# Kernel tuning notes

Measured on AMD Instinct MI355X. Metric: run time of the kernel, lower is better.

## Reference

```python
import jax, jax.numpy as jnp
import numpy as np
import math

CH_IN = 256
NUM_HEADS = 4
HEAD_CH = 64
NUM_GROUPS = 32
EPS = 1e-5


def setup_inputs() -> dict:
    key = jax.random.key(0)
    ks = jax.random.split(key, 12)
    B, C, H, W = 16, CH_IN, 32, 32
    s_in = 1.0 / math.sqrt(C)  # conv 1x1 fan_in init scale
    s_proj = 1.0 / math.sqrt(NUM_HEADS * HEAD_CH)
    return {
        "x": jax.random.normal(ks[0], (B, C, H, W), dtype=jnp.float32),
        "gamma": jnp.ones((C,), dtype=jnp.float32),
        "beta": jnp.zeros((C,), dtype=jnp.float32),
        # per-head 1x1 convs stacked: [num_heads, head_ch, ch_in]
        "wq": jax.random.normal(ks[1], (NUM_HEADS, HEAD_CH, C), dtype=jnp.float32) * s_in,
        "bq": jax.random.normal(ks[2], (NUM_HEADS, HEAD_CH), dtype=jnp.float32) * s_in,
        "wk": jax.random.normal(ks[3], (NUM_HEADS, HEAD_CH, C), dtype=jnp.float32) * s_in,
        "bk": jax.random.normal(ks[4], (NUM_HEADS, HEAD_CH), dtype=jnp.float32) * s_in,
        "wv": jax.random.normal(ks[5], (NUM_HEADS, HEAD_CH, C), dtype=jnp.float32) * s_in,
        "bv": jax.random.normal(ks[6], (NUM_HEADS, HEAD_CH), dtype=jnp.float32) * s_in,
        # output 1x1 conv: [ch_in, num_heads*head_ch]
        "wproj": jax.random.normal(ks[7], (C, NUM_HEADS * HEAD_CH), dtype=jnp.float32) * s_proj,
        "bproj": jax.random.normal(ks[8], (C,), dtype=jnp.float32) * s_proj,
    }


def group_norm(x, gamma, beta):
    B, C, H, W = x.shape
    xg = x.reshape(B, NUM_GROUPS, C // NUM_GROUPS, H, W)
    mean = xg.mean(axis=(2, 3, 4), keepdims=True)
    var = xg.var(axis=(2, 3, 4), keepdims=True)
    xn = (xg - mean) * jax.lax.rsqrt(var + EPS)
    xn = xn.reshape(B, C, H, W)
    return xn * gamma[None, :, None, None] + beta[None, :, None, None]


def reference(x, gamma, beta, wq, bq, wk, bk, wv, bv, wproj, bproj):
    B, C, H, W = x.shape
    L = H * W
    h = group_norm(x, gamma, beta)
    hf = h.reshape(B, C, L)  # [B, C, L]
    # per-head 1x1 convs as batched channel contractions: [B, n_heads, d, L]
    q = jnp.einsum("bcl,ndc->bndl", hf, wq) + bq[None, :, :, None]
    k = jnp.einsum("bcl,ndc->bndl", hf, wk) + bk[None, :, :, None]
    v = jnp.einsum("bcl,ndc->bndl", hf, wv) + bv[None, :, :, None]
    scale = 1.0 / math.sqrt(HEAD_CH)
    scores = jnp.einsum("bndl,bndm->bnlm", q, k) * scale  # [B, n, L, L]
    attn = jax.nn.softmax(scores, axis=-1)
    out = jnp.einsum("bnlm,bndm->bndl", attn, v)  # [B, n, d, L]
    out = out.reshape(B, NUM_HEADS * HEAD_CH, L)  # concat heads along channels
    proj = jnp.einsum("bel,ce->bcl", out, wproj) + bproj[None, :, None]
    return proj.reshape(B, C, H, W) + x
```

## Files before the change

### kernel.cpp

```cpp
#include <hip/hip_runtime.h>
#include <hip/hip_bf16.h>
#include <stdint.h>


typedef __hip_bfloat16 bf16;
typedef __attribute__((ext_vector_type(8))) short short8;
typedef __attribute__((ext_vector_type(4))) float float4v;
typedef __attribute__((ext_vector_type(16))) float float16v;

#if __has_builtin(__builtin_amdgcn_exp2f)
#define EXP2F(x) __builtin_amdgcn_exp2f(x)
#else
#define EXP2F(x) exp2f(x)
#endif

__device__ __forceinline__ float max3f(float a, float b, float c) {
  return fmaxf(fmaxf(a, b), c);
}

__device__ __forceinline__ int qk_fidx(int d, int l) {
  return ((((l >> 5) * 4 + (d >> 4)) * 64 + ((d >> 3) & 1) * 32 + (l & 31)) << 3) + (d & 7);
}
__device__ __forceinline__ int v_fidx(int d, int l) {
  return (((((((l >> 5) * 2 + (d >> 5)) * 2 + ((l >> 4) & 1)) * 2 + ((l >> 3) & 1)) * 32) + (d & 31)) << 3) + (l & 7);
}

__global__ __launch_bounds__(256) void stats_wpack_kernel(
    const float* __restrict__ x, float2* __restrict__ stats,
    const float* __restrict__ wq, const float* __restrict__ wk,
    const float* __restrict__ wv, const float* __restrict__ wp,
    bf16* __restrict__ Wb, bf16* __restrict__ Pb) {
  if (blockIdx.x < 512) {
    int b = blockIdx.x >> 5, g = blockIdx.x & 31;
    const float* xp = x + (size_t)(b * 256 + g * 8) * 1024;
    float s = 0.f, ss = 0.f;
    for (int i = threadIdx.x; i < 8192; i += 256) {
      float v = xp[i]; s += v; ss += v * v;
    }
    #pragma unroll
    for (int o = 32; o; o >>= 1) { s += __shfl_down(s, o); ss += __shfl_down(ss, o); }
    __shared__ float red[2][4];
    int wid = threadIdx.x >> 6;
    if ((threadIdx.x & 63) == 0) { red[0][wid] = s; red[1][wid] = ss; }
    __syncthreads();
    if (threadIdx.x == 0) {
      s  = red[0][0] + red[0][1] + red[0][2] + red[0][3];
      ss = red[1][0] + red[1][1] + red[1][2] + red[1][3];
      float mean = s * (1.f / 8192.f);
      float var  = ss * (1.f / 8192.f) - mean * mean;
      stats[blockIdx.x] = make_float2(mean, rsqrtf(var + 1e-5f));
    }
  } else {
    int i = (blockIdx.x - 512) * 256 + threadIdx.x;
    if (i < 196608) {
      int r = i >> 8, c = i & 255;
      const float* src = (r < 256) ? wq : (r < 512) ? wk : wv;
      Wb[i] = __float2bfloat16(src[(r & 255) * 256 + c]);
    } else {
      int j = i - 196608;
      Pb[j] = __float2bfloat16(wp[j]);
    }
  }
}

__global__ __launch_bounds__(256) void gemm_qkv_fused(
    const float* __restrict__ x, const float* __restrict__ gamma,
    const float* __restrict__ beta, const float2* __restrict__ stats,
    const bf16* __restrict__ Wb,
    const float* __restrict__ bq, const float* __restrict__ bk,
    const float* __restrict__ bv,
    bf16* __restrict__ qkv, size_t qkv_bstride, int b_off) {
  __shared__ bf16 As[128][40];
  __shared__ bf16 Bs[128][40];
  __shared__ float2 ssh[256];
  int zb = blockIdx.z, b = zb + b_off;
  int m0 = blockIdx.y * 128, l0 = blockIdx.x * 128;
  const float* xb = x + (size_t)b * 262144;
  int tid = threadIdx.x, lane = tid & 63, wave = tid >> 6;
  int l16 = lane & 15, quad = lane >> 4;
  int mi0 = (wave & 1) * 4, nj0 = (wave >> 1) * 4;

  {
    float2 st = stats[b * 32 + (tid >> 3)];
    float sc = st.y * gamma[tid];
    ssh[tid] = make_float2(sc, beta[tid] - st.x * sc);
  }

  float4v acc[4][4];
  #pragma unroll
  for (int i = 0; i < 4; i++)
    #pragma unroll
    for (int j = 0; j < 4; j++) acc[i][j] = (float4v){0.f, 0.f, 0.f, 0.f};

  for (int kc = 0; kc < 8; kc++) {
    __syncthreads();
    #pragma unroll
    for (int it = 0; it < 2; it++) {
      int s = it * 256 + tid;
      int mm = s >> 2, kk = (s & 3) * 8;
      *(short8*)&As[mm][kk] = *(const short8*)&Wb[(size_t)(m0 + mm) * 256 + kc * 32 + kk];
    }
    #pragma unroll
    for (int it = 0; it < 16; it++) {
      int i = it * 256 + tid;
      int cl = i >> 7, ll = i & 127;
      float2 sh = ssh[kc * 32 + cl];
      float v = xb[(size_t)(kc * 32 + cl) * 1024 + l0 + ll];
      Bs[ll][cl] = __float2bfloat16(v * sh.x + sh.y);
    }
    __syncthreads();
    short8 af[4], bfr[4];
    #pragma unroll
    for (int i = 0; i < 4; i++) af[i]  = *(const short8*)&As[(mi0 + i) * 16 + l16][quad * 8];
    #pragma unroll
    for (int j = 0; j < 4; j++) bfr[j] = *(const short8*)&Bs[(nj0 + j) * 16 + l16][quad * 8];
    #pragma unroll
    for (int i = 0; i < 4; i++)
      #pragma unroll
      for (int j = 0; j < 4; j++)
        acc[i][j] = __builtin_amdgcn_mfma_f32_16x16x32_bf16(af[i], bfr[j], acc[i][j], 0, 0, 0);
  }

  bf16* Cp = qkv + (size_t)zb * qkv_bstride;
  int sec = m0 >> 8;
  const float* bptr = (sec == 0) ? bq : (sec == 1) ? bk : bv;
  if (sec <= 1) {
    float osc = (sec == 0) ? 0.125f * 1.4426950408889634f : 1.0f;
    bf16* Tp = Cp + sec * 262144;
    #pragma unroll
    for (int i = 0; i < 4; i++) {
      int rrb = (m0 & 255) + (mi0 + i) * 16 + quad * 4;
      int nh = rrb >> 6, d0 = rrb & 63;
      float b0 = bptr[rrb], b1 = bptr[rrb + 1], b2 = bptr[rrb + 2], b3 = bptr[rrb + 3];
      bf16* Tph = Tp + nh * 65536;
      #pragma unroll
      for (int j = 0; j < 4; j++) {
        int l = l0 + (nj0 + j) * 16 + l16;
        bf16 h0 = __float2bfloat16((acc[i][j][0] + b0) * osc);
        bf16 h1 = __float2bfloat16((acc[i][j][1] + b1) * osc);
        bf16 h2 = __float2bfloat16((acc[i][j][2] + b2) * osc);
        bf16 h3 = __float2bfloat16((acc[i][j][3] + b3) * osc);
        uint2 pk;
        pk.x = (unsigned int)*(unsigned short*)&h0 |
               ((unsigned int)*(unsigned short*)&h1 << 16);
        pk.y = (unsigned int)*(unsigned short*)&h2 |
               ((unsigned int)*(unsigned short*)&h3 << 16);
        *(uint2*)&Tph[qk_fidx(d0, l)] = pk;
      }
    }
  } else {
    bf16* Vfp = Cp + 524288;
    #pragma unroll
    for (int i = 0; i < 4; i++)
      #pragma unroll
      for (int r = 0; r < 4; r++) {
        int rr = (m0 & 255) + (mi0 + i) * 16 + quad * 4 + r;
        float bias = bptr[rr];
        int nh = rr >> 6, d = rr & 63;
        bf16* Vfh = Vfp + nh * 65536;
        #pragma unroll
        for (int j = 0; j < 4; j++) {
          int l = l0 + (nj0 + j) * 16 + l16;
          Vfh[v_fidx(d, l)] = __float2bfloat16(acc[i][j][r] + bias);
        }
      }
  }
}

__global__ __launch_bounds__(256) void attn_kernel(
    const bf16* __restrict__ qkv, bf16* __restrict__ oT,
    size_t qkv_bstride, size_t o_bstride) {
  __shared__ __align__(16) float OB[2][2][2176];
  __shared__ float mL[2][2][32], lL[2][2][32];

  int zb, n, gg;
  {
    int f = blockIdx.x + (blockIdx.y << 4) + (blockIdx.z << 6);
    if (gridDim.z == 16) {
      int c = f & 7, r = f >> 3;
      int h = (r >> 4) * 8 + c;
      zb = h >> 2; n = h & 3; gg = r & 15;
    } else {
      zb = blockIdx.z; n = blockIdx.y; gg = blockIdx.x;
    }
  }
  const bf16* base = qkv + (size_t)zb * qkv_bstride;
  const bf16* Qf = base + n * 65536;
  const bf16* Kf = base + 262144 + n * 65536;
  const bf16* Vf = base + 524288 + n * 65536;
  int tid = threadIdx.x;
  int lane = tid & 63, wave = tid >> 6;
  int l31 = lane & 31, hb2 = lane >> 5;
  int qt = wave >> 1, half = wave & 1;
  int g = gg * 2 + qt;
  int q0 = g << 5;

  short8 qb[4];
  #pragma unroll
  for (int ds = 0; ds < 4; ds++)
    qb[ds] = *(const short8*)&Qf[(((g * 4 + ds) << 6) + lane) << 3];

  float m_run = -1e30f, l_run = 0.f;
  float16v oaccT[2];
  #pragma unroll
  for (int dh = 0; dh < 2; dh++)
    #pragma unroll
    for (int r = 0; r < 16; r++) oaccT[dh][r] = 0.f;

  auto swp = [&](unsigned int a, unsigned int b, unsigned int& o0, unsigned int& o1) {
#if __has_builtin(__builtin_amdgcn_permlane32_swap)
    auto rr = __builtin_amdgcn_permlane32_swap((int)a, (int)b, false, false);
    o0 = (unsigned int)rr[0]; o1 = (unsigned int)rr[1];
#else
    unsigned int sa = (unsigned int)__shfl_xor((int)a, 32, 64);
    unsigned int sb = (unsigned int)__shfl_xor((int)b, 32, 64);
    o0 = hb2 ? sb : a;
    o1 = hb2 ? b : sa;
#endif
  };

  int k0 = half << 4;
  for (int kt = k0; kt < k0 + 16; kt++) {
    short8 kf[4];
    #pragma unroll
    for (int ds = 0; ds < 4; ds++)
      kf[ds] = *(const short8*)&Kf[(((kt * 4 + ds) << 6) + lane) << 3];
    short8 vf[2][2];
    #pragma unroll
    for (int dh = 0; dh < 2; dh++)
      #pragma unroll
      for (int s = 0; s < 2; s++)
        vf[dh][s] = *(const short8*)&Vf[((((kt * 2 + dh) * 2 + s) << 6) + lane) << 3];

    float16v sacc;
    #pragma unroll
    for (int r = 0; r < 16; r++) sacc[r] = 0.f;
    #pragma unroll
    for (int ds = 0; ds < 4; ds++)
      sacc = __builtin_amdgcn_mfma_f32_32x32x16_bf16(kf[ds], qb[ds], sacc, 0, 0, 0);

    float a0 = max3f(sacc[0], sacc[1], sacc[2]);
    float a1 = max3f(sacc[3], sacc[4], sacc[5]);
    float a2 = max3f(sacc[6], sacc[7], sacc[8]);
    float a3 = max3f(sacc[9], sacc[10], sacc[11]);
    float a4 = max3f(sacc[12], sacc[13], sacc[14]);
    float cmax = fmaxf(max3f(a0, a1, a2), max3f(a3, a4, sacc[15]));
    cmax = fmaxf(cmax, __shfl_xor(cmax, 32, 64));

    if (__any(cmax > m_run + 8.f)) {
      float mnew = fmaxf(m_run, cmax);
      float alpha = EXP2F(m_run - mnew);
      #pragma unroll
      for (int dh = 0; dh < 2; dh++)
        #pragma unroll
        for (int r = 0; r < 16; r++) oaccT[dh][r] *= alpha;
      l_run *= alpha;
      m_run = mnew;
    }

    float p[16];
    #pragma unroll
    for (int r = 0; r < 16; r++) p[r] = EXP2F(sacc[r] - m_run);
    float s0 = (p[0] + p[1]) + (p[2] + p[3]);
    float s1 = (p[4] + p[5]) + (p[6] + p[7]);
    float s2 = (p[8] + p[9]) + (p[10] + p[11]);
    float s3 = (p[12] + p[13]) + (p[14] + p[15]);
    float psum = (s0 + s1) + (s2 + s3);
    psum += __shfl_xor(psum, 32, 64);
    l_run += psum;

    unsigned int w[8];
    #pragma unroll
    for (int i = 0; i < 8; i++) {
      unsigned int pk;
      asm("v_cvt_pk_bf16_f32 %0, %1, %2" : "=v"(pk) : "v"(p[2 * i]), "v"(p[2 * i + 1]));
      w[i] = pk;
    }
    short8 pb[2];
    {
      unsigned int o0, o1, o2, o3;
      swp(w[0], w[2], o0, o2); swp(w[1], w[3], o1, o3);
      unsigned int* pw = (unsigned int*)&pb[0];
      pw[0] = o0; pw[1] = o1; pw[2] = o2; pw[3] = o3;
      swp(w[4], w[6], o0, o2); swp(w[5], w[7], o1, o3);
      pw = (unsigned int*)&pb[1];
      pw[0] = o0; pw[1] = o1; pw[2] = o2; pw[3] = o3;
    }

    #pragma unroll
    for (int dh = 0; dh < 2; dh++)
      #pragma unroll
      for (int s = 0; s < 2; s++)
        oaccT[dh] = __builtin_amdgcn_mfma_f32_32x32x16_bf16(vf[dh][s], pb[s], oaccT[dh], 0, 0, 0);
  }

  #pragma unroll
  for (int dh = 0; dh < 2; dh++)
    #pragma unroll
    for (int rq = 0; rq < 4; rq++) {
      float4v t = {oaccT[dh][4 * rq], oaccT[dh][4 * rq + 1],
                   oaccT[dh][4 * rq + 2], oaccT[dh][4 * rq + 3]};
      *(float4v*)&OB[half][qt][l31 * 68 + dh * 32 + 8 * rq + 4 * hb2] = t;
    }
  if (hb2 == 0) { mL[half][qt][l31] = m_run; lL[half][qt][l31] = l_run; }
  __syncthreads();

  bf16* op = oT + (size_t)zb * o_bstride + n * 64;
  const float* OA = OB[0][qt];
  const float* OBp = OB[1][qt];
  #pragma unroll
  for (int i = 0; i < 16; i++) {
    int q = (half << 4) + i;
    float mA = mL[0][qt][q], mB = mL[1][qt][q];
    float lA = lL[0][qt][q], lB = lL[1][qt][q];
    float ms = fmaxf(mA, mB);
    float eA = EXP2F(mA - ms), eB = EXP2F(mB - ms);
    float inv = 1.f / (lA * eA + lB * eB);
    float va = OA[q * 68 + lane], vb = OBp[q * 68 + lane];
    float o = (va * eA + vb * eB) * inv;
    op[(size_t)(q0 + q) * 256 + lane] = __float2bfloat16(o);
  }
}

__global__ __launch_bounds__(256) void gemm_proj_mfma(
    const bf16* __restrict__ Pb, const bf16* __restrict__ oT,
    const float* __restrict__ bproj, const float* __restrict__ x,
    float* __restrict__ out, int b_off, size_t o_bstride) {
  __shared__ bf16 As[128][40];
  __shared__ bf16 Bs[128][40];
  int zb = blockIdx.z, b = zb + b_off;
  int m0 = blockIdx.y * 128, l0 = blockIdx.x * 128;
  const bf16* ob = oT + (size_t)zb * o_bstride;
  int tid = threadIdx.x, lane = tid & 63, wave = tid >> 6;
  int l16 = lane & 15, quad = lane >> 4;
  int mi0 = (wave & 1) * 4, nj0 = (wave >> 1) * 4;
  float4v acc[4][4];
  #pragma unroll
  for (int i = 0; i < 4; i++)
    #pragma unroll
    for (int j = 0; j < 4; j++) acc[i][j] = (float4v){0.f, 0.f, 0.f, 0.f};

  for (int kc = 0; kc < 8; kc++) {
    __syncthreads();
    #pragma unroll
    for (int it = 0; it < 2; it++) {
      int s = it * 256 + tid;
      int mm = s >> 2, kk = (s & 3) * 8;
      *(short8*)&As[mm][kk] = *(const short8*)&Pb[(size_t)(m0 + mm) * 256 + kc * 32 + kk];
      *(short8*)&Bs[mm][kk] = *(const short8*)&ob[(size_t)(l0 + mm) * 256 + kc * 32 + kk];
    }
    __syncthreads();
    short8 af[4], bfr[4];
    #pragma unroll
    for (int i = 0; i < 4; i++) af[i]  = *(const short8*)&As[(mi0 + i) * 16 + l16][quad * 8];
    #pragma unroll
    for (int j = 0; j < 4; j++) bfr[j] = *(const short8*)&Bs[(nj0 + j) * 16 + l16][quad * 8];
    #pragma unroll
    for (int i = 0; i < 4; i++)
      #pragma unroll
      for (int j = 0; j < 4; j++)
        acc[i][j] = __builtin_amdgcn_mfma_f32_16x16x32_bf16(af[i], bfr[j], acc[i][j], 0, 0, 0);
  }

  #pragma unroll
  for (int i = 0; i < 4; i++) {
    #pragma unroll
    for (int r = 0; r < 4; r++) {
      int m = m0 + (mi0 + i) * 16 + quad * 4 + r;
      float bias = bproj[m];
      #pragma unroll
      for (int j = 0; j < 4; j++) {
        int l = l0 + (nj0 + j) * 16 + l16;
        size_t idx = (size_t)(b * 256 + m) * 1024 + l;
        out[idx] = acc[i][j][r] + bias + x[idx];
      }
    }
  }
}

extern "C" void kernel_launch(void* const* d_in, const int* in_sizes, int n_in,
                              void* d_out, int out_size, void* d_ws, size_t ws_size,
                              hipStream_t stream) {
  int ix = 0, iga = 1, ibe = 2, iwq = 3, ibq = 4, iwk = 5, ibk = 6,
      iwv = 7, ibv = 8, iwp = 9, ibp = 10;
  if (in_sizes[0] != 4194304) {
    if (in_sizes[10] == 4194304 && in_sizes[1] == 256) {
      ibe = 0; ibk = 1; ibp = 2; ibq = 3; ibv = 4; iga = 5;
      iwk = 6; iwp = 7; iwq = 8; iwv = 9; ix = 10;
    } else if (in_sizes[10] == 4194304 && in_sizes[1] == 65536) {
      ibp = 0; iwp = 1; ibv = 2; iwv = 3; ibk = 4; iwk = 5;
      ibq = 6; iwq = 7; ibe = 8; iga = 9; ix = 10;
    } else {
      for (int i = 0; i < 11; i++) if (in_sizes[i] == 4194304) ix = i;
    }
  }
  const float* x     = (const float*)d_in[ix];
  const float* gamma = (const float*)d_in[iga];
  const float* beta  = (const float*)d_in[ibe];
  const float* wq    = (const float*)d_in[iwq];
  const float* bq    = (const float*)d_in[ibq];
  const float* wk    = (const float*)d_in[iwk];
  const float* bk    = (const float*)d_in[ibk];
  const float* wv    = (const float*)d_in[iwv];
  const float* bv    = (const float*)d_in[ibv];
  const float* wproj = (const float*)d_in[iwp];
  const float* bproj = (const float*)d_in[ibp];
  float* out = (float*)d_out;

  const size_t QKV_B = (size_t)768 * 1024;
  const size_t O_B   = (size_t)256 * 1024;
  char* wsp = (char*)d_ws;
  float2* stats = (float2*)wsp;
  bf16* Wb = (bf16*)(wsp + 8192);
  bf16* Pb = (bf16*)(wsp + 8192 + 393216);
  const size_t OT0 = 8192 + 393216 + 131072;
  size_t full_need = OT0 + (size_t)16 * O_B * 2 + (size_t)16 * QKV_B * 2;

  stats_wpack_kernel<<<1536, 256, 0, stream>>>(x, stats, wq, wk, wv, wproj, Wb, Pb);

  if (ws_size >= full_need) {
    bf16* oT  = (bf16*)(wsp + OT0);
    bf16* qkv = (bf16*)(wsp + OT0 + 16 * O_B * 2);
    gemm_qkv_fused<<<dim3(8, 6, 16), 256, 0, stream>>>(x, gamma, beta, stats, Wb,
                                                       bq, bk, bv, qkv, QKV_B, 0);
    attn_kernel   <<<dim3(16, 4, 16), 256, 0, stream>>>(qkv, oT, QKV_B, O_B);
    gemm_proj_mfma<<<dim3(8, 2, 16), 256, 0, stream>>>(Pb, oT, bproj, x, out, 0, O_B);
  } else {
    bf16* oT  = (bf16*)(wsp + OT0);
    bf16* qkv = (bf16*)(wsp + OT0 + O_B * 2);
    for (int b = 0; b < 16; b++) {
      gemm_qkv_fused<<<dim3(8, 6, 1), 256, 0, stream>>>(x, gamma, beta, stats, Wb,
                                                        bq, bk, bv, qkv, 0, b);
      attn_kernel   <<<dim3(16, 4, 1), 256, 0, stream>>>(qkv, oT, 0, 0);
      gemm_proj_mfma<<<dim3(8, 2, 1), 256, 0, stream>>>(Pb, oT, bproj, x, out, b, 0);
    }
  }
}
```

Baseline: 174.8 us.

## Fuse attention and output projection into one kernel with fragment-packed proj weights

Merges the attention kernel and the projection GEMM. Each 512-thread block handles all four heads for one 32-query tile, combines the two key-half partial softmax results through LDS, and stores the bf16 attention output in LDS. The block then multiplies that output by the projection weights, which are now pre-packed in MFMA fragment order, and adds bias and the residual. This removes the oT round trip through global memory and one kernel launch. In exchange the block is larger, uses more LDS, and loses some parallelism: each block now covers the whole key range with two waves per head, and the grid has fewer, bigger blocks.

```diff
diff --git a/kernel.cpp b/kernel.cpp
--- a/kernel.cpp
+++ b/kernel.cpp
@@ -57,8 +57,12 @@
       const float* src = (r < 256) ? wq : (r < 512) ? wk : wv;
       Wb[i] = __float2bfloat16(src[(r & 255) * 256 + c]);
     } else {
-      int j = i - 196608;
-      Pb[j] = __float2bfloat16(wp[j]);
+      int j2 = i - 196608;
+      int jj = j2 & 7, lane2 = (j2 >> 3) & 63;
+      int kk2 = (j2 >> 9) & 15, w2 = j2 >> 13;
+      int m = w2 * 32 + (lane2 & 31);
+      int e = kk2 * 16 + (lane2 >> 5) * 8 + jj;
+      Pb[j2] = __float2bfloat16(wp[m * 256 + e]);
     }
   }
 }
@@ -167,38 +171,39 @@
   }
 }
 
-__global__ __launch_bounds__(256) void attn_kernel(
-    const bf16* __restrict__ qkv, bf16* __restrict__ oT,
-    size_t qkv_bstride, size_t o_bstride) {
-  __shared__ __align__(16) float OB[2][2][2176];
-  __shared__ float mL[2][2][32], lL[2][2][32];
-
-  int zb, n, gg;
+__global__ __launch_bounds__(512) void attn_proj_kernel(
+    const bf16* __restrict__ qkv, const bf16* __restrict__ PbF,
+    const float* __restrict__ bproj, const float* __restrict__ x,
+    float* __restrict__ out, size_t qkv_bstride, int b_off) {
+  __shared__ __align__(16) char lds[52736];
+  float* OB   = (float*)lds;
+  float* mL   = (float*)(lds + 34816);
+  float* lL   = (float*)(lds + 35328);
+  bf16*  O_lds = (bf16*)(lds + 35840);
+
+  int b, qg;
   {
-    int f = blockIdx.x + (blockIdx.y << 4) + (blockIdx.z << 6);
-    if (gridDim.z == 16) {
-      int c = f & 7, r = f >> 3;
-      int h = (r >> 4) * 8 + c;
-      zb = h >> 2; n = h & 3; gg = r & 15;
+    int f = blockIdx.x;
+    if (gridDim.x == 512) {
+      int c = f & 7, t = f >> 3;
+      b = ((t & 1) << 3) + c; qg = t >> 1;
     } else {
-      zb = blockIdx.z; n = blockIdx.y; gg = blockIdx.x;
-    }
-  }
-  const bf16* base = qkv + (size_t)zb * qkv_bstride;
+      b = b_off; qg = f;
+    }
+  }
+  const bf16* base = qkv + (size_t)(gridDim.x == 512 ? b : 0) * qkv_bstride;
+  int tid = threadIdx.x;
+  int lane = tid & 63, wave = tid >> 6;
+  int l31 = lane & 31, hb2 = lane >> 5;
+  int n = wave & 3, half = wave >> 2;
   const bf16* Qf = base + n * 65536;
   const bf16* Kf = base + 262144 + n * 65536;
   const bf16* Vf = base + 524288 + n * 65536;
-  int tid = threadIdx.x;
-  int lane = tid & 63, wave = tid >> 6;
-  int l31 = lane & 31, hb2 = lane >> 5;
-  int qt = wave >> 1, half = wave & 1;
-  int g = gg * 2 + qt;
-  int q0 = g << 5;
 
   short8 qb[4];
   #pragma unroll
   for (int ds = 0; ds < 4; ds++)
-    qb[ds] = *(const short8*)&Qf[(((g * 4 + ds) << 6) + lane) << 3];
+    qb[ds] = *(const short8*)&Qf[(((qg * 4 + ds) << 6) + lane) << 3];
 
   float m_run = -1e30f, l_run = 0.f;
   float16v oaccT[2];
@@ -207,15 +212,15 @@
     #pragma unroll
     for (int r = 0; r < 16; r++) oaccT[dh][r] = 0.f;
 
-  auto swp = [&](unsigned int a, unsigned int b, unsigned int& o0, unsigned int& o1) {
+  auto swp = [&](unsigned int a, unsigned int bb, unsigned int& o0, unsigned int& o1) {
 #if __has_builtin(__builtin_amdgcn_permlane32_swap)
-    auto rr = __builtin_amdgcn_permlane32_swap((int)a, (int)b, false, false);
+    auto rr = __builtin_amdgcn_permlane32_swap((int)a, (int)bb, false, false);
     o0 = (unsigned int)rr[0]; o1 = (unsigned int)rr[1];
 #else
     unsigned int sa = (unsigned int)__shfl_xor((int)a, 32, 64);
-    unsigned int sb = (unsigned int)__shfl_xor((int)b, 32, 64);
+    unsigned int sb = (unsigned int)__shfl_xor((int)bb, 32, 64);
     o0 = hb2 ? sb : a;
-    o1 = hb2 ? b : sa;
+    o1 = hb2 ? bb : sa;
 #endif
   };
 
@@ -294,87 +299,54 @@
         oaccT[dh] = __builtin_amdgcn_mfma_f32_32x32x16_bf16(vf[dh][s], pb[s], oaccT[dh], 0, 0, 0);
   }
 
-  #pragma unroll
-  for (int dh = 0; dh < 2; dh++)
-    #pragma unroll
-    for (int rq = 0; rq < 4; rq++) {
-      float4v t = {oaccT[dh][4 * rq], oaccT[dh][4 * rq + 1],
-                   oaccT[dh][4 * rq + 2], oaccT[dh][4 * rq + 3]};
-      *(float4v*)&OB[half][qt][l31 * 68 + dh * 32 + 8 * rq + 4 * hb2] = t;
-    }
-  if (hb2 == 0) { mL[half][qt][l31] = m_run; lL[half][qt][l31] = l_run; }
+  if (half == 1) {
+    float* OBn = OB + n * 2176;
+    #pragma unroll
+    for (int dh = 0; dh < 2; dh++)
+      #pragma unroll
+      for (int rq = 0; rq < 4; rq++) {
+        float4v t = {oaccT[dh][4 * rq], oaccT[dh][4 * rq + 1],
+                     oaccT[dh][4 * rq + 2], oaccT[dh][4 * rq + 3]};
+        *(float4v*)&OBn[l31 * 68 + dh * 32 + 8 * rq + 4 * hb2] = t;
+      }
+    if (hb2 == 0) { mL[n * 32 + l31] = m_run; lL[n * 32 + l31] = l_run; }
+  }
   __syncthreads();
-
-  bf16* op = oT + (size_t)zb * o_bstride + n * 64;
-  const float* OA = OB[0][qt];
-  const float* OBp = OB[1][qt];
-  #pragma unroll
-  for (int i = 0; i < 16; i++) {
-    int q = (half << 4) + i;
-    float mA = mL[0][qt][q], mB = mL[1][qt][q];
-    float lA = lL[0][qt][q], lB = lL[1][qt][q];
-    float ms = fmaxf(mA, mB);
-    float eA = EXP2F(mA - ms), eB = EXP2F(mB - ms);
-    float inv = 1.f / (lA * eA + lB * eB);
-    float va = OA[q * 68 + lane], vb = OBp[q * 68 + lane];
-    float o = (va * eA + vb * eB) * inv;
-    op[(size_t)(q0 + q) * 256 + lane] = __float2bfloat16(o);
-  }
-}
-
-__global__ __launch_bounds__(256) void gemm_proj_mfma(
-    const bf16* __restrict__ Pb, const bf16* __restrict__ oT,
-    const float* __restrict__ bproj, const float* __restrict__ x,
-    float* __restrict__ out, int b_off, size_t o_bstride) {
-  __shared__ bf16 As[128][40];
-  __shared__ bf16 Bs[128][40];
-  int zb = blockIdx.z, b = zb + b_off;
-  int m0 = blockIdx.y * 128, l0 = blockIdx.x * 128;
-  const bf16* ob = oT + (size_t)zb * o_bstride;
-  int tid = threadIdx.x, lane = tid & 63, wave = tid >> 6;
-  int l16 = lane & 15, quad = lane >> 4;
-  int mi0 = (wave & 1) * 4, nj0 = (wave >> 1) * 4;
-  float4v acc[4][4];
-  #pragma unroll
-  for (int i = 0; i < 4; i++)
-    #pragma unroll
-    for (int j = 0; j < 4; j++) acc[i][j] = (float4v){0.f, 0.f, 0.f, 0.f};
-
-  for (int kc = 0; kc < 8; kc++) {
-    __syncthreads();
-    #pragma unroll
-    for (int it = 0; it < 2; it++) {
-      int s = it * 256 + tid;
-      int mm = s >> 2, kk = (s & 3) * 8;
-      *(short8*)&As[mm][kk] = *(const short8*)&Pb[(size_t)(m0 + mm) * 256 + kc * 32 + kk];
-      *(short8*)&Bs[mm][kk] = *(const short8*)&ob[(size_t)(l0 + mm) * 256 + kc * 32 + kk];
-    }
-    __syncthreads();
-    short8 af[4], bfr[4];
-    #pragma unroll
-    for (int i = 0; i < 4; i++) af[i]  = *(const short8*)&As[(mi0 + i) * 16 + l16][quad * 8];
-    #pragma unroll
-    for (int j = 0; j < 4; j++) bfr[j] = *(const short8*)&Bs[(nj0 + j) * 16 + l16][quad * 8];
-    #pragma unroll
-    for (int i = 0; i < 4; i++)
-      #pragma unroll
-      for (int j = 0; j < 4; j++)
-        acc[i][j] = __builtin_amdgcn_mfma_f32_16x16x32_bf16(af[i], bfr[j], acc[i][j], 0, 0, 0);
-  }
-
-  #pragma unroll
-  for (int i = 0; i < 4; i++) {
-    #pragma unroll
-    for (int r = 0; r < 4; r++) {
-      int m = m0 + (mi0 + i) * 16 + quad * 4 + r;
-      float bias = bproj[m];
-      #pragma unroll
-      for (int j = 0; j < 4; j++) {
-        int l = l0 + (nj0 + j) * 16 + l16;
-        size_t idx = (size_t)(b * 256 + m) * 1024 + l;
-        out[idx] = acc[i][j][r] + bias + x[idx];
+  if (half == 0) {
+    float mB = mL[n * 32 + l31], lB = lL[n * 32 + l31];
+    float ms = fmaxf(m_run, mB);
+    float eA = EXP2F(m_run - ms), eB = EXP2F(mB - ms);
+    float inv = 1.f / (l_run * eA + lB * eB);
+    eA *= inv; eB *= inv;
+    const float* OBn = OB + n * 2176 + l31 * 68;
+    bf16* orow = O_lds + l31 * 264 + n * 64;
+    #pragma unroll
+    for (int dh = 0; dh < 2; dh++)
+      #pragma unroll
+      for (int r = 0; r < 16; r++) {
+        int d = dh * 32 + (r & 3) + 8 * (r >> 2) + 4 * hb2;
+        orow[d] = __float2bfloat16(oaccT[dh][r] * eA + OBn[d] * eB);
       }
-    }
+  }
+  __syncthreads();
+
+  float16v pacc;
+  #pragma unroll
+  for (int r = 0; r < 16; r++) pacc[r] = 0.f;
+  #pragma unroll
+  for (int kk = 0; kk < 16; kk++) {
+    short8 a = *(const short8*)&O_lds[l31 * 264 + kk * 16 + hb2 * 8];
+    short8 bb = *(const short8*)&PbF[(((wave * 16 + kk) << 6) + lane) << 3];
+    pacc = __builtin_amdgcn_mfma_f32_32x32x16_bf16(a, bb, pacc, 0, 0, 0);
+  }
+  int m = (wave << 5) + l31;
+  float bias = bproj[m];
+  const float* xr = x + (((size_t)(b * 256 + m)) << 10) + (qg << 5);
+  float* orw = out + (((size_t)(b * 256 + m)) << 10) + (qg << 5);
+  #pragma unroll
+  for (int r = 0; r < 16; r++) {
+    int ll = (r & 3) + 8 * (r >> 2) + 4 * hb2;
+    orw[ll] = pacc[r] + bias + xr[ll];
   }
 }
 
@@ -408,31 +380,26 @@
   float* out = (float*)d_out;
 
   const size_t QKV_B = (size_t)768 * 1024;
-  const size_t O_B   = (size_t)256 * 1024;
   char* wsp = (char*)d_ws;
   float2* stats = (float2*)wsp;
   bf16* Wb = (bf16*)(wsp + 8192);
   bf16* Pb = (bf16*)(wsp + 8192 + 393216);
-  const size_t OT0 = 8192 + 393216 + 131072;
-  size_t full_need = OT0 + (size_t)16 * O_B * 2 + (size_t)16 * QKV_B * 2;
+  const size_t QKV0 = 8192 + 393216 + 131072;
+  size_t full_need = QKV0 + (size_t)16 * QKV_B * 2;
 
   stats_wpack_kernel<<<1536, 256, 0, stream>>>(x, stats, wq, wk, wv, wproj, Wb, Pb);
 
   if (ws_size >= full_need) {
-    bf16* oT  = (bf16*)(wsp + OT0);
-    bf16* qkv = (bf16*)(wsp + OT0 + 16 * O_B * 2);
+    bf16* qkv = (bf16*)(wsp + QKV0);
     gemm_qkv_fused<<<dim3(8, 6, 16), 256, 0, stream>>>(x, gamma, beta, stats, Wb,
                                                        bq, bk, bv, qkv, QKV_B, 0);
-    attn_kernel   <<<dim3(16, 4, 16), 256, 0, stream>>>(qkv, oT, QKV_B, O_B);
-    gemm_proj_mfma<<<dim3(8, 2, 16), 256, 0, stream>>>(Pb, oT, bproj, x, out, 0, O_B);
+    attn_proj_kernel<<<512, 512, 0, stream>>>(qkv, Pb, bproj, x, out, QKV_B, 0);
   } else {
-    bf16* oT  = (bf16*)(wsp + OT0);
-    bf16* qkv = (bf16*)(wsp + OT0 + O_B * 2);
+    bf16* qkv = (bf16*)(wsp + QKV0);
     for (int b = 0; b < 16; b++) {
       gemm_qkv_fused<<<dim3(8, 6, 1), 256, 0, stream>>>(x, gamma, beta, stats, Wb,
                                                         bq, bk, bv, qkv, 0, b);
-      attn_kernel   <<<dim3(16, 4, 1), 256, 0, stream>>>(qkv, oT, 0, 0);
-      gemm_proj_mfma<<<dim3(8, 2, 1), 256, 0, stream>>>(Pb, oT, bproj, x, out, b, 0);
-    }
-  }
-}
+      attn_proj_kernel<<<32, 512, 0, stream>>>(qkv, Pb, bproj, x, out, 0, b);
+    }
+  }
+}
```

After: 153.1 us. 12.4% less time.
